# Optimization experiments

Hardware: AMD Instinct MI355X
Metric: run time of the kernel (lower is better)

Reference implementation:

```python
import jax, jax.numpy as jnp
import numpy as np

B, S, H, D = 8, 4096, 32, 128
DM = H * D

def setup_inputs() -> dict:
    key = jax.random.key(0)
    k1, k2, k3, k4, k5 = jax.random.split(key, 5)
    return {
        "hidden_state": jax.random.normal(k1, (B, DM), dtype=jnp.float32),
        "key_states": jax.random.normal(k2, (B, S, DM), dtype=jnp.float32),
        "value_states": jax.random.normal(k3, (B, S, DM), dtype=jnp.float32),
        "Wq": jax.random.normal(k4, (DM, DM), dtype=jnp.float32) * 0.02,
        "bq": jax.random.normal(k5, (DM,), dtype=jnp.float32) * 0.02,
    }

def reference(hidden_state, key_states, value_states, Wq, bq):
    # q projection: torch Linear -> x @ W^T + b
    q = (hidden_state @ Wq.T + bq).reshape(B, H, D)          # [B,H,D]
    k = key_states.reshape(B, S, H, D)                        # [B,S,H,D]
    v = value_states.reshape(B, S, H, D)
    # NOTE: original module applies no 1/sqrt(D) scaling
    scores = jnp.einsum('bhd,bshd->bhs', q, k)                # [B,H,S]
    probs = jax.nn.softmax(scores, axis=-1)
    out = jnp.einsum('bhs,bshd->bhd', probs, v)               # [B,H,D]
    return out[:, :, None, :]                                 # [B,H,1,D] to match torch output
```

## Files before the change

kernel.cpp:

```cpp
#include <hip/hip_runtime.h>

#define B 8
#define S 4096
#define H 32
#define D 128
#define DM 4096

#define SPLIT 4
#define SC (S / SPLIT)
#define NT 512
#define NWAVE 8
#define PSTR 132

__global__ __launch_bounds__(256) void qproj_kernel(
    const float* __restrict__ hidden, const float* __restrict__ Wq,
    const float* __restrict__ bq, float* __restrict__ qout)
{
    const int lane = threadIdx.x & 63;
    const int wave = threadIdx.x >> 6;
    const int j = blockIdx.x * 4 + wave;

    const float4* __restrict__ w   = (const float4*)(Wq + (size_t)j * DM);
    const float4* __restrict__ hid = (const float4*)hidden;

    float a[B];
#pragma unroll
    for (int b = 0; b < B; ++b) a[b] = 0.f;

#pragma unroll 4
    for (int i = 0; i < DM / (4 * 64); ++i) {
        const int idx = lane + 64 * i;
        const float4 wv = w[idx];
#pragma unroll
        for (int b = 0; b < B; ++b) {
            const float4 hv = hid[b * (DM / 4) + idx];
            a[b] += wv.x * hv.x + wv.y * hv.y + wv.z * hv.z + wv.w * hv.w;
        }
    }
#pragma unroll
    for (int b = 0; b < B; ++b) {
#pragma unroll
        for (int mk = 1; mk <= 32; mk <<= 1) a[b] += __shfl_xor(a[b], mk);
    }
    if (lane == 0) {
        const float bias = bq[j];
#pragma unroll
        for (int b = 0; b < B; ++b) qout[b * DM + j] = a[b] + bias;
    }
}

__global__ __launch_bounds__(NT) void attn_partial(
    const float* __restrict__ kptr, const float* __restrict__ vptr,
    const float* __restrict__ qws, float* __restrict__ part)
{
    __shared__ float sc[SC];
    __shared__ float red[NWAVE];
    __shared__ float outp[NWAVE][D];

    const int tid  = threadIdx.x;
    const int lane = tid & 63;
    const int wave = tid >> 6;
    const int gid  = tid >> 5;
    const int g    = lane >> 5;
    const int l    = lane & 31;
    const int c    = blockIdx.x & (SPLIT - 1);
    const int h    = (blockIdx.x >> 2) & (H - 1);
    const int b    = blockIdx.x >> 7;

    const size_t base = (((size_t)b * S + (size_t)c * SC) * H + h) * D;
    const float* kb = kptr + base;
    const float* vb = vptr + base;

    const float4 q4 = *(const float4*)(qws + (size_t)b * DM + h * D + 4 * l);

#pragma unroll 4
    for (int it = 0; it < SC / 16; ++it) {
        const int s = it * 16 + gid;
        const float4 k4 = *(const float4*)(kb + (size_t)s * DM + 4 * l);
        float p = q4.x * k4.x + q4.y * k4.y + q4.z * k4.z + q4.w * k4.w;
        p += __shfl_xor(p, 16);
        p += __shfl_xor(p, 8);
        p += __shfl_xor(p, 4);
        p += __shfl_xor(p, 2);
        p += __shfl_xor(p, 1);
        if (l == 0) sc[s] = p;
    }
    __syncthreads();

    float m = -3.4e38f;
#pragma unroll
    for (int i = tid; i < SC; i += NT) m = fmaxf(m, sc[i]);
#pragma unroll
    for (int mk = 1; mk <= 32; mk <<= 1) m = fmaxf(m, __shfl_xor(m, mk));
    if (lane == 0) red[wave] = m;
    __syncthreads();
    float M = red[0];
#pragma unroll
    for (int w = 1; w < NWAVE; ++w) M = fmaxf(M, red[w]);

    float lsum = 0.f;
#pragma unroll
    for (int i = tid; i < SC; i += NT) {
        const float e = __expf(sc[i] - M);
        sc[i] = e;
        lsum += e;
    }
#pragma unroll
    for (int mk = 1; mk <= 32; mk <<= 1) lsum += __shfl_xor(lsum, mk);
    __syncthreads();
    if (lane == 0) red[wave] = lsum;
    __syncthreads();
    float tot = 0.f;
#pragma unroll
    for (int w = 0; w < NWAVE; ++w) tot += red[w];

    float4 acc = make_float4(0.f, 0.f, 0.f, 0.f);
    const int s0 = wave * (SC / NWAVE);
#pragma unroll 4
    for (int i = 0; i < SC / NWAVE; i += 2) {
        const int s = s0 + i + g;
        const float p = sc[s];
        const float4 v4 = *(const float4*)(vb + (size_t)s * DM + 4 * l);
        acc.x += p * v4.x;
        acc.y += p * v4.y;
        acc.z += p * v4.z;
        acc.w += p * v4.w;
    }
    acc.x += __shfl_xor(acc.x, 32);
    acc.y += __shfl_xor(acc.y, 32);
    acc.z += __shfl_xor(acc.z, 32);
    acc.w += __shfl_xor(acc.w, 32);
    if (g == 0) *(float4*)(&outp[wave][4 * l]) = acc;
    __syncthreads();

    float* rec = part + ((size_t)(b * H + h) * SPLIT + c) * PSTR;
    if (tid < D) {
        float r = 0.f;
#pragma unroll
        for (int w = 0; w < NWAVE; ++w) r += outp[w][tid];
        rec[tid] = r;
    } else if (tid == D) {
        rec[D] = M;
        rec[D + 1] = tot;
    }
}

__global__ __launch_bounds__(128) void combine_kernel(
    const float* __restrict__ part, float* __restrict__ out)
{
    const int bh = blockIdx.x;
    const int d  = threadIdx.x;
    const float* rec = part + (size_t)bh * SPLIT * PSTR;

    float M = -3.4e38f;
#pragma unroll
    for (int c = 0; c < SPLIT; ++c) M = fmaxf(M, rec[c * PSTR + D]);
    float denom = 0.f, o = 0.f;
#pragma unroll
    for (int c = 0; c < SPLIT; ++c) {
        const float w = __expf(rec[c * PSTR + D] - M);
        denom += w * rec[c * PSTR + D + 1];
        o     += w * rec[c * PSTR + d];
    }
    out[(size_t)bh * D + d] = o / denom;
}

extern "C" void kernel_launch(void* const* d_in, const int* in_sizes, int n_in,
                              void* d_out, int out_size, void* d_ws, size_t ws_size,
                              hipStream_t stream)
{
    const float* hidden = (const float*)d_in[0];
    const float* keys   = (const float*)d_in[1];
    const float* vals   = (const float*)d_in[2];
    const float* Wq     = (const float*)d_in[3];
    const float* bq     = (const float*)d_in[4];
    float* outp = (float*)d_out;
    float* qws  = (float*)d_ws;
    float* part = qws + (size_t)B * DM;

    qproj_kernel<<<DM / 4, 256, 0, stream>>>(hidden, Wq, bq, qws);
    attn_partial<<<B * H * SPLIT, NT, 0, stream>>>(keys, vals, qws, part);
    combine_kernel<<<B * H, 128, 0, stream>>>(part, outp);
}
```

Before: 219.5 us.

## Process all heads per sequence chunk for contiguous full-row K/V reads

The attention partial kernel is reorganized so each block handles one batch and a 64-position chunk across all 32 heads. Each 32-lane group owns one head, so every K/V row of the full model width is read contiguously instead of as per-head 512-byte slices. This removes most block-wide barriers and reductions, since softmax stats are computed per group with shuffles. In exchange the combine kernel must merge 64 partials per (batch, head) instead of 4, and the partial workspace grows accordingly.

```diff
diff --git a/kernel.cpp b/kernel.cpp
--- a/kernel.cpp
+++ b/kernel.cpp
@@ -6,10 +6,9 @@
 #define D 128
 #define DM 4096
 
-#define SPLIT 4
-#define SC (S / SPLIT)
-#define NT 512
-#define NWAVE 8
+#define CS 64
+#define NCHUNK (S / CS)
+#define NT 1024
 #define PSTR 132
 
 __global__ __launch_bounds__(256) void qproj_kernel(
@@ -49,100 +48,63 @@
     }
 }
 
-__global__ __launch_bounds__(NT) void attn_partial(
+__global__ __launch_bounds__(NT, 8) void attn_partial(
     const float* __restrict__ kptr, const float* __restrict__ vptr,
     const float* __restrict__ qws, float* __restrict__ part)
 {
-    __shared__ float sc[SC];
-    __shared__ float red[NWAVE];
-    __shared__ float outp[NWAVE][D];
+    __shared__ float sc[H][CS + 1];
 
-    const int tid  = threadIdx.x;
-    const int lane = tid & 63;
-    const int wave = tid >> 6;
-    const int gid  = tid >> 5;
-    const int g    = lane >> 5;
-    const int l    = lane & 31;
-    const int c    = blockIdx.x & (SPLIT - 1);
-    const int h    = (blockIdx.x >> 2) & (H - 1);
-    const int b    = blockIdx.x >> 7;
+    const int tid = threadIdx.x;
+    const int g   = tid >> 5;
+    const int l   = tid & 31;
+    const int c   = blockIdx.x & (NCHUNK - 1);
+    const int b   = blockIdx.x >> 6;
 
-    const size_t base = (((size_t)b * S + (size_t)c * SC) * H + h) * D;
-    const float* kb = kptr + base;
-    const float* vb = vptr + base;
+    const size_t base = ((size_t)b * S + (size_t)c * CS) * DM;
+    const float4* __restrict__ kb = (const float4*)(kptr + base);
+    const float4* __restrict__ vb = (const float4*)(vptr + base);
 
-    const float4 q4 = *(const float4*)(qws + (size_t)b * DM + h * D + 4 * l);
+    const float4 q4 = *(const float4*)(qws + (size_t)b * DM + 4 * tid);
 
 #pragma unroll 4
-    for (int it = 0; it < SC / 16; ++it) {
-        const int s = it * 16 + gid;
-        const float4 k4 = *(const float4*)(kb + (size_t)s * DM + 4 * l);
+    for (int s = 0; s < CS; ++s) {
+        const float4 k4 = kb[(size_t)s * (DM / 4) + tid];
         float p = q4.x * k4.x + q4.y * k4.y + q4.z * k4.z + q4.w * k4.w;
+        p += __shfl_xor(p, 1);
+        p += __shfl_xor(p, 2);
+        p += __shfl_xor(p, 4);
+        p += __shfl_xor(p, 8);
         p += __shfl_xor(p, 16);
-        p += __shfl_xor(p, 8);
-        p += __shfl_xor(p, 4);
-        p += __shfl_xor(p, 2);
-        p += __shfl_xor(p, 1);
-        if (l == 0) sc[s] = p;
+        if (l == 0) sc[g][s] = p;
     }
-    __syncthreads();
 
-    float m = -3.4e38f;
+    const float s0v = sc[g][l];
+    const float s1v = sc[g][l + 32];
+    float m = fmaxf(s0v, s1v);
 #pragma unroll
-    for (int i = tid; i < SC; i += NT) m = fmaxf(m, sc[i]);
+    for (int mk = 1; mk <= 16; mk <<= 1) m = fmaxf(m, __shfl_xor(m, mk));
+    const float e0 = __expf(s0v - m);
+    const float e1 = __expf(s1v - m);
+    float sum = e0 + e1;
 #pragma unroll
-    for (int mk = 1; mk <= 32; mk <<= 1) m = fmaxf(m, __shfl_xor(m, mk));
-    if (lane == 0) red[wave] = m;
-    __syncthreads();
-    float M = red[0];
-#pragma unroll
-    for (int w = 1; w < NWAVE; ++w) M = fmaxf(M, red[w]);
-
-    float lsum = 0.f;
-#pragma unroll
-    for (int i = tid; i < SC; i += NT) {
-        const float e = __expf(sc[i] - M);
-        sc[i] = e;
-        lsum += e;
-    }
-#pragma unroll
-    for (int mk = 1; mk <= 32; mk <<= 1) lsum += __shfl_xor(lsum, mk);
-    __syncthreads();
-    if (lane == 0) red[wave] = lsum;
-    __syncthreads();
-    float tot = 0.f;
-#pragma unroll
-    for (int w = 0; w < NWAVE; ++w) tot += red[w];
+    for (int mk = 1; mk <= 16; mk <<= 1) sum += __shfl_xor(sum, mk);
+    sc[g][l]      = e0;
+    sc[g][l + 32] = e1;
 
     float4 acc = make_float4(0.f, 0.f, 0.f, 0.f);
-    const int s0 = wave * (SC / NWAVE);
 #pragma unroll 4
-    for (int i = 0; i < SC / NWAVE; i += 2) {
-        const int s = s0 + i + g;
-        const float p = sc[s];
-        const float4 v4 = *(const float4*)(vb + (size_t)s * DM + 4 * l);
+    for (int s = 0; s < CS; ++s) {
+        const float p = sc[g][s];
+        const float4 v4 = vb[(size_t)s * (DM / 4) + tid];
         acc.x += p * v4.x;
         acc.y += p * v4.y;
         acc.z += p * v4.z;
         acc.w += p * v4.w;
     }
-    acc.x += __shfl_xor(acc.x, 32);
-    acc.y += __shfl_xor(acc.y, 32);
-    acc.z += __shfl_xor(acc.z, 32);
-    acc.w += __shfl_xor(acc.w, 32);
-    if (g == 0) *(float4*)(&outp[wave][4 * l]) = acc;
-    __syncthreads();
 
-    float* rec = part + ((size_t)(b * H + h) * SPLIT + c) * PSTR;
-    if (tid < D) {
-        float r = 0.f;
-#pragma unroll
-        for (int w = 0; w < NWAVE; ++w) r += outp[w][tid];
-        rec[tid] = r;
-    } else if (tid == D) {
-        rec[D] = M;
-        rec[D + 1] = tot;
-    }
+    float* rec = part + ((size_t)(b * H + g) * NCHUNK + c) * PSTR;
+    *(float4*)(rec + 4 * l) = acc;
+    if (l == 0) { rec[D] = m; rec[D + 1] = sum; }
 }
 
 __global__ __launch_bounds__(128) void combine_kernel(
@@ -150,14 +112,14 @@
 {
     const int bh = blockIdx.x;
     const int d  = threadIdx.x;
-    const float* rec = part + (size_t)bh * SPLIT * PSTR;
+    const float* rec = part + (size_t)bh * NCHUNK * PSTR;
 
     float M = -3.4e38f;
-#pragma unroll
-    for (int c = 0; c < SPLIT; ++c) M = fmaxf(M, rec[c * PSTR + D]);
+#pragma unroll 8
+    for (int c = 0; c < NCHUNK; ++c) M = fmaxf(M, rec[c * PSTR + D]);
     float denom = 0.f, o = 0.f;
-#pragma unroll
-    for (int c = 0; c < SPLIT; ++c) {
+#pragma unroll 8
+    for (int c = 0; c < NCHUNK; ++c) {
         const float w = __expf(rec[c * PSTR + D] - M);
         denom += w * rec[c * PSTR + D + 1];
         o     += w * rec[c * PSTR + d];
@@ -179,6 +141,6 @@
     float* part = qws + (size_t)B * DM;
 
     qproj_kernel<<<DM / 4, 256, 0, stream>>>(hidden, Wq, bq, qws);
-    attn_partial<<<B * H * SPLIT, NT, 0, stream>>>(keys, vals, qws, part);
+    attn_partial<<<B * NCHUNK, NT, 0, stream>>>(keys, vals, qws, part);
     combine_kernel<<<B * H, 128, 0, stream>>>(part, outp);
 }
```

Measured after the change: 238.9 us. +8.8%, slower.
